# Optimization experiments

Measured on AMD Instinct MI355X. Metric: run time of the kernel, lower is better.

The kernel has to match this reference:

```python
import jax, jax.numpy as jnp
import numpy as np

N = 50000      # nodes
DEG = 16       # avg degree
E = N * DEG    # edges
FIN = 128
FQK = 64
FV = 64
H = 8


def setup_inputs() -> dict:
    key = jax.random.key(0)
    k1, k2, k3, k4 = jax.random.split(key, 4)
    x = jax.random.normal(k1, (N, FIN), dtype=jnp.float32)
    # torch Linear(Fin, 2*Fqk+Fv, bias=False); stored here as [Fin, Ftot] so y = x @ W
    W = jax.random.normal(k2, (FIN, 2 * FQK + FV), dtype=jnp.float32) / np.sqrt(FIN)
    # edges: src sorted and covering all nodes (required by scatter_softmax semantics)
    src = jnp.repeat(jnp.arange(N, dtype=jnp.int32), DEG)
    dest = jax.random.randint(k3, (E,), 0, N, dtype=jnp.int32)
    ei = jnp.stack([src, dest])  # [2, E]
    batch = jnp.sort(jax.random.randint(k4, (N,), 0, 64, dtype=jnp.int32))
    return {"x": x, "W": W, "batch": batch, "ei": ei}


def reference(x, W, batch, ei):
    n = x.shape[0]
    Fh = FQK // H   # per-head qk dim
    Fhv = FV // H   # per-head v dim
    scaling = float(Fh) ** (-0.5)

    qkv = x @ W  # [N, 2*Fqk+Fv]
    q, k, v = jnp.split(qkv, [FQK, 2 * FQK], axis=-1)
    q = (q * scaling).reshape(n, H, Fh)
    k = k.reshape(n, H, Fh)
    v = v.reshape(n, H, Fhv)

    src, dest = ei[0], ei[1]
    qs = q[src]   # [E, H, Fh]
    ks = k[dest]  # [E, H, Fh]
    vs = v[dest]  # [E, H, Fhv]

    aw = jnp.einsum("ehf,ehf->eh", qs, ks)  # per-edge per-head logits

    # segment softmax over src (numerically stable, same math as exp/segsum(exp))
    amax = jax.ops.segment_max(aw, src, num_segments=n)
    ex = jnp.exp(aw - amax[src])
    denom = jax.ops.segment_sum(ex, src, num_segments=n)
    aw = ex / denom[src]  # [E, H]

    out = jax.ops.segment_sum(aw[:, :, None] * vs, src, num_segments=n)  # [N, H, Fhv]
    return out.reshape(n, H * Fhv)
```

## Files before the change

### kernel.cpp

```cpp
#include <hip/hip_runtime.h>
#include <math.h>

#define N_NODES 50000
#define DEG 16
#define E_EDGES (N_NODES * DEG)
#define FIN 128
#define FTOT 192
#define FQK 64
#define FV 64
#define H 8

typedef __attribute__((ext_vector_type(8))) short short8;
typedef __attribute__((ext_vector_type(4))) float float4v;

__device__ inline unsigned short f2bf(float f) {
    unsigned int u = __float_as_uint(f);
    unsigned int r = u + 0x7fffu + ((u >> 16) & 1u);
    return (unsigned short)(r >> 16);
}
__device__ inline float bf2f(unsigned short b) {
    return __uint_as_float(((unsigned int)b) << 16);
}
__device__ inline float bflo(unsigned int w) { return __uint_as_float(w << 16); }
__device__ inline float bfhi(unsigned int w) { return __uint_as_float(w & 0xffff0000u); }

#define LDB 136
#define LDC 194

__global__ void wt_prep(const float* __restrict__ W, unsigned short* __restrict__ Wt) {
    int t = blockIdx.x * 256 + threadIdx.x;
    if (t >= FIN * FTOT) return;
    int k = t / FTOT, n = t % FTOT;
    Wt[n * LDB + k] = f2bf(W[t]);
}

__global__ __launch_bounds__(256) void gemm_qkv(const float* __restrict__ x,
                                                const unsigned short* __restrict__ Wt,
                                                unsigned short* __restrict__ qkv) {
    __shared__ unsigned short Bt[FTOT * LDB];
    unsigned short* Ct = Bt;
    const int tid = threadIdx.x;

#pragma unroll
    for (int i = 0; i < 13; i++) {
        int c = tid + i * 256;
        if (c < (FTOT * LDB) / 8)
            *(uint4*)(&Bt[c * 8]) = *(const uint4*)(Wt + c * 8);
    }

    const int wave = tid >> 6, lane = tid & 63;
    const int m = lane & 15, q = lane >> 4;
    const int row = blockIdx.x * 64 + wave * 16 + m;
    const int rowc = min(row, N_NODES - 1);

    short8 a[4];
    const float* xr = x + rowc * FIN;
#pragma unroll
    for (int s = 0; s < 4; s++) {
        float4v f0 = *(const float4v*)(xr + s * 32 + q * 8);
        float4v f1 = *(const float4v*)(xr + s * 32 + q * 8 + 4);
        short8 av;
        av[0] = (short)f2bf(f0.x); av[1] = (short)f2bf(f0.y);
        av[2] = (short)f2bf(f0.z); av[3] = (short)f2bf(f0.w);
        av[4] = (short)f2bf(f1.x); av[5] = (short)f2bf(f1.y);
        av[6] = (short)f2bf(f1.z); av[7] = (short)f2bf(f1.w);
        a[s] = av;
    }
    __syncthreads();

    float4v acc[12];
#pragma unroll
    for (int ct = 0; ct < 12; ct++) acc[ct] = (float4v){0.f, 0.f, 0.f, 0.f};
#pragma unroll
    for (int ct = 0; ct < 12; ct++) {
#pragma unroll
        for (int s = 0; s < 4; s++) {
            short8 b = *(const short8*)(&Bt[(ct * 16 + m) * LDB + s * 32 + q * 8]);
            acc[ct] = __builtin_amdgcn_mfma_f32_16x16x32_bf16(a[s], b, acc[ct], 0, 0, 0);
        }
    }
    __syncthreads();

    const int lrow0 = wave * 16 + q * 4;
#pragma unroll
    for (int ct = 0; ct < 12; ct++) {
        const int col = ct * 16 + m;
        int off; float scale;
        if (col < FQK)          { off = col;                      scale = 0.35355339059327373f; }
        else if (col < 2 * FQK) { off = 64 + 2 * (col - 64);      scale = 1.f; }
        else                    { off = 64 + 2 * (col - 128) + 1; scale = 1.f; }
#pragma unroll
        for (int i = 0; i < 4; i++)
            Ct[(lrow0 + i) * LDC + off] = f2bf(acc[ct][i] * scale);
    }
    __syncthreads();

    unsigned int* qg = (unsigned int*)qkv;
    const int base = blockIdx.x * 64;
#pragma unroll
    for (int i = 0; i < 24; i++) {
        int l = tid + i * 256;
        int r = l / 96, dw = l - r * 96;
        if (base + r < N_NODES)
            qg[(size_t)(base + r) * 96 + dw] = *(const unsigned int*)(&Ct[r * LDC + 2 * dw]);
    }
}

__global__ __launch_bounds__(256) void attn(const unsigned short* __restrict__ qkv,
                                            const int* __restrict__ dest,
                                            float* __restrict__ out) {
    const int node = blockIdx.x * 4 + (threadIdx.x >> 6);
    const int lane = threadIdx.x & 63;
    const int quarter = lane >> 4;
    const int l = lane & 15;
    if (node >= N_NODES) return;

    const uint2 qw = *(const uint2*)(qkv + node * FTOT + 4 * l);
    const float q0 = bflo(qw.x), q1 = bfhi(qw.x) ;
    const float q2 = bflo(qw.y), q3 = bfhi(qw.y);

    const int4 dd = ((const int4*)(dest + (size_t)node * DEG))[quarter];

    uint4 kv[4];
    {
        const int d0 = dd.x, d1 = dd.y, d2 = dd.z, d3 = dd.w;
        kv[0] = *(const uint4*)(qkv + d0 * FTOT + 64 + 8 * l);
        kv[1] = *(const uint4*)(qkv + d1 * FTOT + 64 + 8 * l);
        kv[2] = *(const uint4*)(qkv + d2 * FTOT + 64 + 8 * l);
        kv[3] = *(const uint4*)(qkv + d3 * FTOT + 64 + 8 * l);
    }

    float lg[4];
#pragma unroll
    for (int t = 0; t < 4; t++) {
        float p = q0 * bflo(kv[t].x);
        p = fmaf(q1, bflo(kv[t].y), p);
        p = fmaf(q2, bflo(kv[t].z), p);
        p = fmaf(q3, bflo(kv[t].w), p);
        p += __shfl_xor(p, 1, 64);
        lg[t] = p;
    }

    float m = fmaxf(fmaxf(lg[0], lg[1]), fmaxf(lg[2], lg[3]));
    m = fmaxf(m, __shfl_xor(m, 16, 64));
    m = fmaxf(m, __shfl_xor(m, 32, 64));

    float s = 0.f, o0 = 0.f, o1 = 0.f, o2 = 0.f, o3 = 0.f;
#pragma unroll
    for (int t = 0; t < 4; t++) {
        const float p = __expf(lg[t] - m);
        s += p;
        o0 = fmaf(p, bfhi(kv[t].x), o0);
        o1 = fmaf(p, bfhi(kv[t].y), o1);
        o2 = fmaf(p, bfhi(kv[t].z), o2);
        o3 = fmaf(p, bfhi(kv[t].w), o3);
    }
    s  += __shfl_xor(s, 16, 64);  s  += __shfl_xor(s, 32, 64);
    o0 += __shfl_xor(o0, 16, 64); o0 += __shfl_xor(o0, 32, 64);
    o1 += __shfl_xor(o1, 16, 64); o1 += __shfl_xor(o1, 32, 64);
    o2 += __shfl_xor(o2, 16, 64); o2 += __shfl_xor(o2, 32, 64);
    o3 += __shfl_xor(o3, 16, 64); o3 += __shfl_xor(o3, 32, 64);

    if (quarter == 0) {
        const float inv = 1.0f / s;
        float4 r; r.x = o0 * inv; r.y = o1 * inv; r.z = o2 * inv; r.w = o3 * inv;
        *(float4*)(out + node * 64 + 4 * l) = r;
    }
}

extern "C" void kernel_launch(void* const* d_in, const int* in_sizes, int n_in,
                              void* d_out, int out_size, void* d_ws, size_t ws_size,
                              hipStream_t stream) {
    const float* x = (const float*)d_in[0];
    const float* W = (const float*)d_in[1];
    const int* ei = (const int*)d_in[3];
    const int* dest = ei + E_EDGES;
    float* out = (float*)d_out;

    unsigned short* qkv = (unsigned short*)d_ws;
    unsigned short* Wt  = (unsigned short*)((char*)d_ws + 19200000);

    wt_prep<<<(FIN * FTOT + 255) / 256, 256, 0, stream>>>(W, Wt);
    gemm_qkv<<<(N_NODES + 63) / 64, 256, 0, stream>>>(x, Wt, qkv);
    attn<<<(N_NODES + 3) / 4, 256, 0, stream>>>(qkv, dest, out);
}
```

Baseline: 114.1 us.

## Map one node per 16-lane quarter-wave in attention, each lane processing all 16 edges

```diff
diff --git a/kernel.cpp b/kernel.cpp
--- a/kernel.cpp
+++ b/kernel.cpp
@@ -17,9 +17,6 @@
     unsigned int u = __float_as_uint(f);
     unsigned int r = u + 0x7fffu + ((u >> 16) & 1u);
     return (unsigned short)(r >> 16);
-}
-__device__ inline float bf2f(unsigned short b) {
-    return __uint_as_float(((unsigned int)b) << 16);
 }
 __device__ inline float bflo(unsigned int w) { return __uint_as_float(w << 16); }
 __device__ inline float bfhi(unsigned int w) { return __uint_as_float(w & 0xffff0000u); }
@@ -109,63 +106,52 @@
 __global__ __launch_bounds__(256) void attn(const unsigned short* __restrict__ qkv,
                                             const int* __restrict__ dest,
                                             float* __restrict__ out) {
-    const int node = blockIdx.x * 4 + (threadIdx.x >> 6);
-    const int lane = threadIdx.x & 63;
-    const int quarter = lane >> 4;
-    const int l = lane & 15;
-    if (node >= N_NODES) return;
+    const int tid = threadIdx.x;
+    const int wave = tid >> 6, lane = tid & 63;
+    const int quarter = lane >> 4, l = lane & 15;
+    const int node = (blockIdx.x * 4 + wave) * 4 + quarter;
 
+    const int dd = dest[(size_t)node * DEG + l];
     const uint2 qw = *(const uint2*)(qkv + node * FTOT + 4 * l);
-    const float q0 = bflo(qw.x), q1 = bfhi(qw.x) ;
+
+    uint4 kv[DEG];
+#pragma unroll
+    for (int e = 0; e < DEG; e++) {
+        const int d = __shfl(dd, (lane & 48) + e, 64);
+        kv[e] = *(const uint4*)(qkv + d * FTOT + 64 + 8 * l);
+    }
+
+    const float q0 = bflo(qw.x), q1 = bfhi(qw.x);
     const float q2 = bflo(qw.y), q3 = bfhi(qw.y);
 
-    const int4 dd = ((const int4*)(dest + (size_t)node * DEG))[quarter];
-
-    uint4 kv[4];
-    {
-        const int d0 = dd.x, d1 = dd.y, d2 = dd.z, d3 = dd.w;
-        kv[0] = *(const uint4*)(qkv + d0 * FTOT + 64 + 8 * l);
-        kv[1] = *(const uint4*)(qkv + d1 * FTOT + 64 + 8 * l);
-        kv[2] = *(const uint4*)(qkv + d2 * FTOT + 64 + 8 * l);
-        kv[3] = *(const uint4*)(qkv + d3 * FTOT + 64 + 8 * l);
+    float lg[DEG];
+#pragma unroll
+    for (int e = 0; e < DEG; e++) {
+        float p = q0 * bflo(kv[e].x);
+        p = fmaf(q1, bflo(kv[e].y), p);
+        p = fmaf(q2, bflo(kv[e].z), p);
+        p = fmaf(q3, bflo(kv[e].w), p);
+        p += __shfl_xor(p, 1, 64);
+        lg[e] = p;
     }
 
-    float lg[4];
+    float m = lg[0];
 #pragma unroll
-    for (int t = 0; t < 4; t++) {
-        float p = q0 * bflo(kv[t].x);
-        p = fmaf(q1, bflo(kv[t].y), p);
-        p = fmaf(q2, bflo(kv[t].z), p);
-        p = fmaf(q3, bflo(kv[t].w), p);
-        p += __shfl_xor(p, 1, 64);
-        lg[t] = p;
-    }
-
-    float m = fmaxf(fmaxf(lg[0], lg[1]), fmaxf(lg[2], lg[3]));
-    m = fmaxf(m, __shfl_xor(m, 16, 64));
-    m = fmaxf(m, __shfl_xor(m, 32, 64));
+    for (int e = 1; e < DEG; e++) m = fmaxf(m, lg[e]);
 
     float s = 0.f, o0 = 0.f, o1 = 0.f, o2 = 0.f, o3 = 0.f;
 #pragma unroll
-    for (int t = 0; t < 4; t++) {
-        const float p = __expf(lg[t] - m);
+    for (int e = 0; e < DEG; e++) {
+        const float p = __expf(lg[e] - m);
         s += p;
-        o0 = fmaf(p, bfhi(kv[t].x), o0);
-        o1 = fmaf(p, bfhi(kv[t].y), o1);
-        o2 = fmaf(p, bfhi(kv[t].z), o2);
-        o3 = fmaf(p, bfhi(kv[t].w), o3);
+        o0 = fmaf(p, bfhi(kv[e].x), o0);
+        o1 = fmaf(p, bfhi(kv[e].y), o1);
+        o2 = fmaf(p, bfhi(kv[e].z), o2);
+        o3 = fmaf(p, bfhi(kv[e].w), o3);
     }
-    s  += __shfl_xor(s, 16, 64);  s  += __shfl_xor(s, 32, 64);
-    o0 += __shfl_xor(o0, 16, 64); o0 += __shfl_xor(o0, 32, 64);
-    o1 += __shfl_xor(o1, 16, 64); o1 += __shfl_xor(o1, 32, 64);
-    o2 += __shfl_xor(o2, 16, 64); o2 += __shfl_xor(o2, 32, 64);
-    o3 += __shfl_xor(o3, 16, 64); o3 += __shfl_xor(o3, 32, 64);
-
-    if (quarter == 0) {
-        const float inv = 1.0f / s;
-        float4 r; r.x = o0 * inv; r.y = o1 * inv; r.z = o2 * inv; r.w = o3 * inv;
-        *(float4*)(out + node * 64 + 4 * l) = r;
-    }
+    const float inv = 1.0f / s;
+    float4v r; r.x = o0 * inv; r.y = o1 * inv; r.z = o2 * inv; r.w = o3 * inv;
+    *(float4v*)(out + (size_t)node * 64 + 4 * l) = r;
 }
 
 extern "C" void kernel_launch(void* const* d_in, const int* in_sizes, int n_in,
@@ -182,5 +168,5 @@
 
     wt_prep<<<(FIN * FTOT + 255) / 256, 256, 0, stream>>>(W, Wt);
     gemm_qkv<<<(N_NODES + 63) / 64, 256, 0, stream>>>(x, Wt, qkv);
-    attn<<<(N_NODES + 3) / 4, 256, 0, stream>>>(qkv, dest, out);
+    attn<<<N_NODES / 16, 256, 0, stream>>>(qkv, dest, out);
 }
```

New measurement: 117.3 us. +2.8%, slower.
